# Optimization experiments

Hardware: AMD Instinct MI355X
Metric: run time of the kernel (lower is better)

Reference implementation:

```python
import jax, jax.numpy as jnp
import numpy as np

B, N, HID = 4, 2048, 1024
QKV, NH = 1024, 16
HD = QKV // NH


def setup_inputs() -> dict:
    key = jax.random.key(0)
    ks = jax.random.split(key, 5)
    s = 1.0 / np.sqrt(HID)
    x = jax.random.normal(ks[0], (B, N, HID), dtype=jnp.float32)
    Wq = jax.random.normal(ks[1], (HID, QKV), dtype=jnp.float32) * s
    Wk = jax.random.normal(ks[2], (HID, QKV), dtype=jnp.float32) * s
    Wv = jax.random.normal(ks[3], (HID, QKV), dtype=jnp.float32) * s
    Wo = jax.random.normal(ks[4], (QKV, HID), dtype=jnp.float32) * (1.0 / np.sqrt(QKV))
    return {"x": x, "Wq": Wq, "Wk": Wk, "Wv": Wv, "Wo": Wo}


def reference(x, Wq, Wk, Wv, Wo):
    # Projections: [B, N, QKV]
    q = x @ Wq
    k = x @ Wk
    v = x @ Wv
    # Split heads -> [B, NH, N, HD]
    def split(t):
        return t.reshape(B, N, NH, HD).transpose(0, 2, 1, 3)
    q, k, v = split(q), split(k), split(v)
    # NOTE: original scales by 1/sqrt(qkv_dim) (full dim), not head_dim
    q = q * (1.0 / jnp.sqrt(jnp.float32(QKV)))
    scores = jnp.einsum("bhqd,bhkd->bhqk", q, k)  # [B, NH, N, N]
    attn = jax.nn.softmax(scores, axis=-1)
    out = jnp.einsum("bhqk,bhkd->bhqd", attn, v)  # [B, NH, N, HD]
    out = out.transpose(0, 2, 1, 3).reshape(B, N, QKV)
    return out @ Wo
```

## Files before the change

### kernel.cpp

```cpp
#include <hip/hip_runtime.h>

typedef unsigned short u16;
typedef unsigned int u32;
typedef __attribute__((ext_vector_type(8))) short bf16x8;
typedef __attribute__((ext_vector_type(4))) float f32x4;
typedef __attribute__((ext_vector_type(16))) float f32x16;

#define L2E 1.44269504088896340736f

__device__ __forceinline__ u16 f2bf(float f) {
  unsigned u = __float_as_uint(f);
  u += 0x7FFF + ((u >> 16) & 1u);
  return (u16)(u >> 16);
}

__device__ __forceinline__ u32 cvtpk(float lo, float hi) {
  u32 r;
  asm("v_cvt_pk_bf16_f32 %0, %1, %2" : "=v"(r) : "v"(lo), "v"(hi));
  return r;
}

__device__ __forceinline__ void gload_lds16(const u16* g, u16* lds) {
  __builtin_amdgcn_global_load_lds(
      (const __attribute__((address_space(1))) void*)g,
      (__attribute__((address_space(3))) void*)lds, 16, 0, 0);
}

__global__ __launch_bounds__(256) void k_cvt(const float* __restrict__ in,
                                             u16* __restrict__ out) {
  const int i = (blockIdx.x * 256 + threadIdx.x) * 4;
  float4 a = *(const float4*)(in + i);
  ushort4 o;
  o.x = f2bf(a.x); o.y = f2bf(a.y); o.z = f2bf(a.z); o.w = f2bf(a.w);
  *(ushort4*)(out + i) = o;
}

__global__ __launch_bounds__(256) void k_tw(
    const float* __restrict__ w0, const float* __restrict__ w1,
    const float* __restrict__ w2, const float* __restrict__ w3,
    u16* __restrict__ o0, u16* __restrict__ o1,
    u16* __restrict__ o2, u16* __restrict__ o3) {
  __shared__ float t[64][65];
  const float* W = blockIdx.z == 0 ? w0 : blockIdx.z == 1 ? w1 : blockIdx.z == 2 ? w2 : w3;
  u16* O = blockIdx.z == 0 ? o0 : blockIdx.z == 1 ? o1 : blockIdx.z == 2 ? o2 : o3;
  const int nb = blockIdx.x * 64, kb = blockIdx.y * 64;
  const int lx = threadIdx.x & 63, ly = threadIdx.x >> 6;
  for (int r = ly; r < 64; r += 4)
    t[r][lx] = W[(size_t)(kb + r) * 1024 + nb + lx];
  __syncthreads();
  for (int r = ly; r < 64; r += 4)
    O[(size_t)(nb + r) * 1024 + kb + lx] = f2bf(t[lx][r]);
}

__device__ __forceinline__ void gemm_core(const u16* __restrict__ Ag,
                                          const u16* __restrict__ Bg,
                                          f32x4 acc[4][4]) {
  __shared__ u16 As[4096], Bs[4096];
  const int tid = threadIdx.x;
  const int lane = tid & 63, wv = tid >> 6;
  const size_t row0 = (size_t)blockIdx.y * 128;
  const size_t col0 = (size_t)blockIdx.x * 128;
  const int rA0 = wv * 32 + (lane >> 2);
  const int rA1 = rA0 + 16;
  const int kk = (lane & 3) * 8;
  const int wr = (wv >> 1) * 64, wc = (wv & 1) * 64;
  const int fr = lane & 15, fk = (lane >> 4) * 8;
#pragma unroll
  for (int m = 0; m < 4; m++)
#pragma unroll
    for (int n = 0; n < 4; n++)
      acc[m][n] = {0.f, 0.f, 0.f, 0.f};

  for (int kt = 0; kt < 32; kt++) {
    const int k0 = kt * 32;
    gload_lds16(Ag + (row0 + rA0) * 1024 + k0 + kk, &As[(wv * 2 + 0) * 512]);
    gload_lds16(Ag + (row0 + rA1) * 1024 + k0 + kk, &As[(wv * 2 + 1) * 512]);
    gload_lds16(Bg + (col0 + rA0) * 1024 + k0 + kk, &Bs[(wv * 2 + 0) * 512]);
    gload_lds16(Bg + (col0 + rA1) * 1024 + k0 + kk, &Bs[(wv * 2 + 1) * 512]);
    __syncthreads();
    bf16x8 af[4], bfr[4];
#pragma unroll
    for (int m = 0; m < 4; m++)
      af[m] = *(const bf16x8*)&As[(wr + m * 16 + fr) * 32 + fk];
#pragma unroll
    for (int n = 0; n < 4; n++)
      bfr[n] = *(const bf16x8*)&Bs[(wc + n * 16 + fr) * 32 + fk];
#pragma unroll
    for (int m = 0; m < 4; m++)
#pragma unroll
      for (int n = 0; n < 4; n++)
        acc[m][n] = __builtin_amdgcn_mfma_f32_16x16x32_bf16(af[m], bfr[n], acc[m][n], 0, 0, 0);
    __syncthreads();
  }
}

__global__ __launch_bounds__(256) void k_proj(
    const u16* __restrict__ xb, const u16* __restrict__ wqT,
    const u16* __restrict__ wkT, const u16* __restrict__ wvT,
    u16* __restrict__ q, u16* __restrict__ k, u16* __restrict__ v) {
  f32x4 acc[4][4];
  const int z = blockIdx.z;
  const u16* Bg = z == 0 ? wqT : z == 1 ? wkT : wvT;
  gemm_core(xb, Bg, acc);
  const int lane = threadIdx.x & 63, wv = threadIdx.x >> 6;
  const int wr = (wv >> 1) * 64, wc = (wv & 1) * 64;
  const int rb = blockIdx.y * 128 + wr + ((lane >> 4) * 4);
  const int cb = blockIdx.x * 128 + wc + (lane & 15);
#pragma unroll
  for (int m = 0; m < 4; m++) {
#pragma unroll
    for (int n = 0; n < 4; n++) {
      const int C = cb + n * 16;
      const int h = C >> 6, d = C & 63;
      if (z == 2) {
        const int R = rb + m * 16;
        const int b = R >> 11, nn = R & 2047;
        const int bh = b * 16 + h;
        ushort4 o;
        o.x = f2bf(acc[m][n][0]); o.y = f2bf(acc[m][n][1]);
        o.z = f2bf(acc[m][n][2]); o.w = f2bf(acc[m][n][3]);
        const size_t off = (size_t)bh * 131072 + (size_t)(nn >> 6) * 4096 +
                           ((nn & 63) >> 3) * 512 + d * 8 + (nn & 7);
        *(ushort4*)&v[off] = o;
      } else if (z == 1) {
#pragma unroll
        for (int i = 0; i < 4; i++) {
          const int R = rb + m * 16 + i;
          const int b = R >> 11, nn = R & 2047;
          const int bh = b * 16 + h;
          const size_t off = (size_t)bh * 131072 + (size_t)(nn >> 6) * 4096 +
                             (d >> 3) * 512 + (nn & 63) * 8 + (d & 7);
          k[off] = f2bf(acc[m][n][i]);
        }
      } else {
        const float s = 0.03125f * L2E;
#pragma unroll
        for (int i = 0; i < 4; i++) {
          const int R = rb + m * 16 + i;
          const int b = R >> 11, nn = R & 2047;
          q[(size_t)((b * 16 + h) * 2048 + nn) * 64 + d] = f2bf(acc[m][n][i] * s);
        }
      }
    }
  }
}

__global__ __launch_bounds__(256) void k_out(const u16* __restrict__ att,
                                             const u16* __restrict__ woT,
                                             float* __restrict__ out) {
  f32x4 acc[4][4];
  gemm_core(att, woT, acc);
  const int lane = threadIdx.x & 63, wv = threadIdx.x >> 6;
  const int wr = (wv >> 1) * 64, wc = (wv & 1) * 64;
  const int rb = blockIdx.y * 128 + wr + ((lane >> 4) * 4);
  const int cb = blockIdx.x * 128 + wc + (lane & 15);
#pragma unroll
  for (int m = 0; m < 4; m++)
#pragma unroll
    for (int n = 0; n < 4; n++)
#pragma unroll
      for (int i = 0; i < 4; i++)
        out[(size_t)(rb + m * 16 + i) * 1024 + cb + n * 16] = acc[m][n][i];
}

__global__ __launch_bounds__(256, 2) void k_attn(const u16* __restrict__ qg,
                                                 const u16* __restrict__ kg,
                                                 const u16* __restrict__ vg,
                                                 u16* __restrict__ att) {
  __shared__ u16 SM[16384];
  const int tid = threadIdx.x;
  const int lane = tid & 63, wv = tid >> 6;
  const int lo5 = lane & 31, hi = lane >> 5;
  const int bh = blockIdx.y;
  const int b = bh >> 4, h = bh & 15;
  const int q0w = blockIdx.x * 128 + wv * 32;
  const size_t qbase = (size_t)bh * 2048 * 64;
  const u16* kt0 = kg + (size_t)bh * 131072;
  const u16* vt0 = vg + (size_t)bh * 131072;

  bf16x8 qb[4];
  {
    const u16* qp = qg + qbase + (size_t)(q0w + lo5) * 64 + hi * 8;
#pragma unroll
    for (int db = 0; db < 4; db++) qb[db] = *(const bf16x8*)(qp + db * 16);
  }

  f32x16 o0, o1;
#pragma unroll
  for (int i = 0; i < 16; i++) { o0[i] = 0.f; o1[i] = 0.f; }
  float m_run = -3.0e38f;
  float l16[16];
#pragma unroll
  for (int i = 0; i < 16; i++) l16[i] = 0.f;

  gload_lds16(kt0 + (size_t)tid * 8, SM + wv * 512);
  gload_lds16(kt0 + (size_t)(256 + tid) * 8, SM + 2048 + wv * 512);
  gload_lds16(vt0 + (size_t)tid * 8, SM + 4096 + wv * 512);
  gload_lds16(vt0 + (size_t)(256 + tid) * 8, SM + 6144 + wv * 512);
  __syncthreads();

  int cur = 0;
  for (int t = 0; t < 32; t++) {
    {
      const int nt = (t + 1) & 31;
      const u16* ks = kt0 + (size_t)nt * 4096;
      const u16* vs = vt0 + (size_t)nt * 4096;
      u16* Kd = SM + (cur ^ 1) * 8192;
      gload_lds16(ks + (size_t)tid * 8, Kd + wv * 512);
      gload_lds16(ks + (size_t)(256 + tid) * 8, Kd + 2048 + wv * 512);
      gload_lds16(vs + (size_t)tid * 8, Kd + 4096 + wv * 512);
      gload_lds16(vs + (size_t)(256 + tid) * 8, Kd + 6144 + wv * 512);
    }

    const u16* Kc = SM + cur * 8192 + hi * 512 + lo5 * 8;
    const u16* Vc = Kc + 4096;

    f32x16 s0, s1;
#pragma unroll
    for (int i = 0; i < 16; i++) { s0[i] = 0.f; s1[i] = 0.f; }
    __builtin_amdgcn_s_setprio(1);
#pragma unroll
    for (int db = 0; db < 4; db++) {
      const bf16x8 k0 = *(const bf16x8*)&Kc[db * 1024];
      const bf16x8 k1 = *(const bf16x8*)&Kc[db * 1024 + 256];
      s0 = __builtin_amdgcn_mfma_f32_32x32x16_bf16(k0, qb[db], s0, 0, 0, 0);
      s1 = __builtin_amdgcn_mfma_f32_32x32x16_bf16(k1, qb[db], s1, 0, 0, 0);
    }
    __builtin_amdgcn_s_setprio(0);

    float tmx[16];
#pragma unroll
    for (int i = 0; i < 16; i++) tmx[i] = fmaxf(s0[i], s1[i]);
#pragma unroll
    for (int off = 8; off; off >>= 1)
#pragma unroll
      for (int i = 0; i < off; i++) tmx[i] = fmaxf(tmx[i], tmx[i + off]);
    const float tmax = fmaxf(tmx[0], __shfl_xor(tmx[0], 32, 64));

    const bool skip = __all(tmax - m_run <= 8.0f);
    if (!skip) {
      const float mnew = fmaxf(m_run, tmax);
      const float sc = __builtin_amdgcn_exp2f(m_run - mnew);
      m_run = mnew;
#pragma unroll
      for (int i = 0; i < 16; i++) {
        l16[i] *= sc; o0[i] *= sc; o1[i] *= sc;
      }
    }

    float p0[16], p1[16];
#pragma unroll
    for (int i = 0; i < 16; i++) {
      p0[i] = __builtin_amdgcn_exp2f(s0[i] - m_run);
      p1[i] = __builtin_amdgcn_exp2f(s1[i] - m_run);
      l16[i] += p0[i] + p1[i];
    }

    bf16x8 pa[4];
#pragma unroll
    for (int kh = 0; kh < 2; kh++) {
      const float* pp = kh ? p1 : p0;
#pragma unroll
      for (int kl = 0; kl < 2; kl++) {
        const int r0 = kl * 8;
        const u32 a0 = cvtpk(pp[r0 + 0], pp[r0 + 1]);
        const u32 a1 = cvtpk(pp[r0 + 2], pp[r0 + 3]);
        const u32 b0 = cvtpk(pp[r0 + 4], pp[r0 + 5]);
        const u32 b1 = cvtpk(pp[r0 + 6], pp[r0 + 7]);
        const u32 a0x = (u32)__shfl_xor((int)a0, 32, 64);
        const u32 a1x = (u32)__shfl_xor((int)a1, 32, 64);
        const u32 b0x = (u32)__shfl_xor((int)b0, 32, 64);
        const u32 b1x = (u32)__shfl_xor((int)b1, 32, 64);
        union { u32 w[4]; bf16x8 v; } U;
        U.w[0] = hi ? b0x : a0;
        U.w[1] = hi ? b1x : a1;
        U.w[2] = hi ? b0 : a0x;
        U.w[3] = hi ? b1 : a1x;
        pa[kh * 2 + kl] = U.v;
      }
    }

    __builtin_amdgcn_s_setprio(1);
#pragma unroll
    for (int ks = 0; ks < 4; ks++) {
      const bf16x8 v0 = *(const bf16x8*)&Vc[ks * 1024];
      const bf16x8 v1 = *(const bf16x8*)&Vc[ks * 1024 + 256];
      o0 = __builtin_amdgcn_mfma_f32_32x32x16_bf16(v0, pa[ks], o0, 0, 0, 0);
      o1 = __builtin_amdgcn_mfma_f32_32x32x16_bf16(v1, pa[ks], o1, 0, 0, 0);
    }
    __builtin_amdgcn_s_setprio(0);

    __syncthreads();
    cur ^= 1;
  }

  float ls[8];
#pragma unroll
  for (int i = 0; i < 8; i++) ls[i] = l16[i] + l16[i + 8];
#pragma unroll
  for (int off = 4; off; off >>= 1)
#pragma unroll
    for (int i = 0; i < off; i++) ls[i] += ls[i + off];
  const float lsum = ls[0] + __shfl_xor(ls[0], 32, 64);
  const float linv = 1.0f / lsum;

  u16* W = SM + wv * 2176;
#pragma unroll
  for (int r = 0; r < 16; r++) {
    const int dd = (r & 3) + 8 * (r >> 2) + 4 * hi;
    W[lo5 * 68 + dd] = f2bf(o0[r] * linv);
    W[lo5 * 68 + 32 + dd] = f2bf(o1[r] * linv);
  }
  const int q_loc = lane >> 1, dh = (lane & 1) * 32;
  u16* dst = att + (size_t)(b * 2048 + q0w + q_loc) * 1024 + h * 64 + dh;
#pragma unroll
  for (int c = 0; c < 4; c++) {
    bf16x8 val = *(const bf16x8*)&W[q_loc * 68 + dh + c * 8];
    *(bf16x8*)(dst + c * 8) = val;
  }
}

extern "C" void kernel_launch(void* const* d_in, const int* in_sizes, int n_in,
                              void* d_out, int out_size, void* d_ws, size_t ws_size,
                              hipStream_t stream) {
  const float* x  = (const float*)d_in[0];
  const float* Wq = (const float*)d_in[1];
  const float* Wk = (const float*)d_in[2];
  const float* Wv = (const float*)d_in[3];
  const float* Wo = (const float*)d_in[4];
  float* out = (float*)d_out;

  char* ws = (char*)d_ws;
  u16* xb  = (u16*)ws; ws += (size_t)8192 * 1024 * 2;
  u16* wqT = (u16*)ws; ws += (size_t)1024 * 1024 * 2;
  u16* wkT = (u16*)ws; ws += (size_t)1024 * 1024 * 2;
  u16* wvT = (u16*)ws; ws += (size_t)1024 * 1024 * 2;
  u16* woT = (u16*)ws; ws += (size_t)1024 * 1024 * 2;
  u16* qb  = (u16*)ws; ws += (size_t)8192 * 1024 * 2;
  u16* kb  = (u16*)ws; ws += (size_t)8192 * 1024 * 2;
  u16* vb  = (u16*)ws; ws += (size_t)8192 * 1024 * 2;
  u16* att = (u16*)ws; ws += (size_t)8192 * 1024 * 2;

  k_cvt<<<dim3(8192), dim3(256), 0, stream>>>(x, xb);
  k_tw<<<dim3(16, 16, 4), dim3(256), 0, stream>>>(Wq, Wk, Wv, Wo, wqT, wkT, wvT, woT);
  k_proj<<<dim3(8, 64, 3), dim3(256), 0, stream>>>(xb, wqT, wkT, wvT, qb, kb, vb);
  k_attn<<<dim3(16, 64), dim3(256), 0, stream>>>(qb, kb, vb, att);
  k_out<<<dim3(8, 64), dim3(256), 0, stream>>>(att, woT, out);
}
```

Baseline: 316.5 us.

## Rewrite projection and output GEMMs with pre-tiled operands and triple-buffered LDS pipeline

Adds a templated GEMM kernel with 512 threads and 128x256 tiles. It reads operands that the cvt, weight-transpose and attention-output kernels now write directly in a K-blocked tile layout, so each 16-byte global-to-LDS load is contiguous. A three-stage LDS ring replaces the synchronous load-barrier-compute loop, prefetching two k-steps ahead with waitcnt and barrier tuning and setprio around the MFMAs. This is meant to hide global-load latency and cut per-iteration barrier stalls in both GEMMs. In exchange it uses more LDS per block and gives a less flexible data layout.

Measured after the change: 283.9 us. 10.3% less time.

```diff
diff --git a/kernel.cpp b/kernel.cpp
--- a/kernel.cpp
+++ b/kernel.cpp
@@ -8,6 +8,7 @@
 
 #define L2E 1.44269504088896340736f
 
+
 __device__ __forceinline__ u16 f2bf(float f) {
   unsigned u = __float_as_uint(f);
   u += 0x7FFF + ((u >> 16) & 1u);
@@ -29,138 +30,172 @@
 __global__ __launch_bounds__(256) void k_cvt(const float* __restrict__ in,
                                              u16* __restrict__ out) {
   const int i = (blockIdx.x * 256 + threadIdx.x) * 4;
+  const int n = i >> 10, kk = i & 1023;
   float4 a = *(const float4*)(in + i);
   ushort4 o;
   o.x = f2bf(a.x); o.y = f2bf(a.y); o.z = f2bf(a.z); o.w = f2bf(a.w);
-  *(ushort4*)(out + i) = o;
+  const size_t off = (size_t)(kk >> 5) * 262144 + (size_t)(n >> 7) * 4096 +
+                     ((kk >> 3) & 3) * 1024 + (n & 127) * 8 + (kk & 7);
+  *(ushort4*)(out + off) = o;
 }
 
 __global__ __launch_bounds__(256) void k_tw(
     const float* __restrict__ w0, const float* __restrict__ w1,
     const float* __restrict__ w2, const float* __restrict__ w3,
-    u16* __restrict__ o0, u16* __restrict__ o1,
-    u16* __restrict__ o2, u16* __restrict__ o3) {
+    u16* __restrict__ wqkv, u16* __restrict__ wo) {
   __shared__ float t[64][65];
-  const float* W = blockIdx.z == 0 ? w0 : blockIdx.z == 1 ? w1 : blockIdx.z == 2 ? w2 : w3;
-  u16* O = blockIdx.z == 0 ? o0 : blockIdx.z == 1 ? o1 : blockIdx.z == 2 ? o2 : o3;
+  const int z = blockIdx.z;
+  const float* W = z == 0 ? w0 : z == 1 ? w1 : z == 2 ? w2 : w3;
   const int nb = blockIdx.x * 64, kb = blockIdx.y * 64;
   const int lx = threadIdx.x & 63, ly = threadIdx.x >> 6;
   for (int r = ly; r < 64; r += 4)
     t[r][lx] = W[(size_t)(kb + r) * 1024 + nb + lx];
   __syncthreads();
-  for (int r = ly; r < 64; r += 4)
-    O[(size_t)(nb + r) * 1024 + kb + lx] = f2bf(t[lx][r]);
-}
-
-__device__ __forceinline__ void gemm_core(const u16* __restrict__ Ag,
-                                          const u16* __restrict__ Bg,
-                                          f32x4 acc[4][4]) {
-  __shared__ u16 As[4096], Bs[4096];
-  const int tid = threadIdx.x;
-  const int lane = tid & 63, wv = tid >> 6;
-  const size_t row0 = (size_t)blockIdx.y * 128;
-  const size_t col0 = (size_t)blockIdx.x * 128;
-  const int rA0 = wv * 32 + (lane >> 2);
-  const int rA1 = rA0 + 16;
-  const int kk = (lane & 3) * 8;
-  const int wr = (wv >> 1) * 64, wc = (wv & 1) * 64;
-  const int fr = lane & 15, fk = (lane >> 4) * 8;
+  const int kk = kb + lx;
+  for (int r = ly; r < 64; r += 4) {
+    const int n = nb + r;
+    const u16 val = f2bf(t[lx][r]);
+    if (z < 3) {
+      const size_t off = (size_t)(kk >> 5) * 98304 + (size_t)(z * 8 + (n >> 7)) * 4096 +
+                         ((kk >> 3) & 3) * 1024 + (n & 127) * 8 + (kk & 7);
+      wqkv[off] = val;
+    } else {
+      const size_t off = (size_t)(kk >> 5) * 32768 + (size_t)(n >> 7) * 4096 +
+                         ((kk >> 3) & 3) * 1024 + (n & 127) * 8 + (kk & 7);
+      wo[off] = val;
+    }
+  }
+}
+
+template <int MODE>
+__global__ __launch_bounds__(512) void k_mm(const u16* __restrict__ Ag,
+                                            const u16* __restrict__ Bg,
+                                            u16* __restrict__ qo,
+                                            u16* __restrict__ ko,
+                                            u16* __restrict__ vo,
+                                            float* __restrict__ outp) {
+  __shared__ u16 SM[3 * 12288];
+  const int tid = threadIdx.x, lane = tid & 63, wv = tid >> 6;
+  const int wm = wv >> 2, wn = wv & 3;
+  const int fr = lane & 15, hi = lane >> 4;
+  const int bn = blockIdx.x, bm = blockIdx.y;
+  const int PKB = (MODE == 0) ? 98304 : 32768;
+  const u16* Asrc = Ag + (size_t)bm * 4096;
+  const u16* Bsrc = Bg + (size_t)(bn * 2) * 4096;
+
+  f32x4 acc[4][4];
 #pragma unroll
   for (int m = 0; m < 4; m++)
 #pragma unroll
-    for (int n = 0; n < 4; n++)
-      acc[m][n] = {0.f, 0.f, 0.f, 0.f};
-
-  for (int kt = 0; kt < 32; kt++) {
-    const int k0 = kt * 32;
-    gload_lds16(Ag + (row0 + rA0) * 1024 + k0 + kk, &As[(wv * 2 + 0) * 512]);
-    gload_lds16(Ag + (row0 + rA1) * 1024 + k0 + kk, &As[(wv * 2 + 1) * 512]);
-    gload_lds16(Bg + (col0 + rA0) * 1024 + k0 + kk, &Bs[(wv * 2 + 0) * 512]);
-    gload_lds16(Bg + (col0 + rA1) * 1024 + k0 + kk, &Bs[(wv * 2 + 1) * 512]);
-    __syncthreads();
+    for (int n = 0; n < 4; n++) acc[m][n] = {0.f, 0.f, 0.f, 0.f};
+
+  int aoff[4], boff[4];
+#pragma unroll
+  for (int m = 0; m < 4; m++)
+    aoff[m] = hi * 1024 + (wm * 64 + m * 16 + fr) * 8;
+#pragma unroll
+  for (int n = 0; n < 4; n++) {
+    const int col = wn * 64 + n * 16 + fr;
+    boff[n] = 4096 + (col >> 7) * 4096 + hi * 1024 + (col & 127) * 8;
+  }
+
+#pragma unroll
+  for (int p = 0; p < 2; p++) {
+    u16* D = SM + p * 12288;
+    const u16* As = Asrc + (size_t)p * 262144;
+    const u16* Bs = Bsrc + (size_t)p * PKB;
+    gload_lds16(As + tid * 8, D + wv * 512);
+    gload_lds16(Bs + tid * 8, D + 4096 + wv * 512);
+    gload_lds16(Bs + 4096 + tid * 8, D + 8192 + wv * 512);
+  }
+  asm volatile("s_waitcnt vmcnt(3)" ::: "memory");
+  __builtin_amdgcn_s_barrier();
+  __builtin_amdgcn_sched_barrier(0);
+
+  int cur = 0, stg = 2;
+  for (int t = 0; t < 32; t++) {
+    {
+      const int nt = (t + 2) & 31;
+      u16* D = SM + stg * 12288;
+      const u16* As = Asrc + (size_t)nt * 262144;
+      const u16* Bs = Bsrc + (size_t)nt * PKB;
+      gload_lds16(As + tid * 8, D + wv * 512);
+      gload_lds16(Bs + tid * 8, D + 4096 + wv * 512);
+      gload_lds16(Bs + 4096 + tid * 8, D + 8192 + wv * 512);
+    }
+    const u16* buf = SM + cur * 12288;
     bf16x8 af[4], bfr[4];
 #pragma unroll
-    for (int m = 0; m < 4; m++)
-      af[m] = *(const bf16x8*)&As[(wr + m * 16 + fr) * 32 + fk];
-#pragma unroll
-    for (int n = 0; n < 4; n++)
-      bfr[n] = *(const bf16x8*)&Bs[(wc + n * 16 + fr) * 32 + fk];
+    for (int m = 0; m < 4; m++) af[m] = *(const bf16x8*)&buf[aoff[m]];
+#pragma unroll
+    for (int n = 0; n < 4; n++) bfr[n] = *(const bf16x8*)&buf[boff[n]];
+    asm volatile("s_waitcnt lgkmcnt(0)" ::: "memory");
+    __builtin_amdgcn_sched_barrier(0);
+    __builtin_amdgcn_s_setprio(1);
 #pragma unroll
     for (int m = 0; m < 4; m++)
 #pragma unroll
       for (int n = 0; n < 4; n++)
         acc[m][n] = __builtin_amdgcn_mfma_f32_16x16x32_bf16(af[m], bfr[n], acc[m][n], 0, 0, 0);
-    __syncthreads();
-  }
-}
-
-__global__ __launch_bounds__(256) void k_proj(
-    const u16* __restrict__ xb, const u16* __restrict__ wqT,
-    const u16* __restrict__ wkT, const u16* __restrict__ wvT,
-    u16* __restrict__ q, u16* __restrict__ k, u16* __restrict__ v) {
-  f32x4 acc[4][4];
-  const int z = blockIdx.z;
-  const u16* Bg = z == 0 ? wqT : z == 1 ? wkT : wvT;
-  gemm_core(xb, Bg, acc);
-  const int lane = threadIdx.x & 63, wv = threadIdx.x >> 6;
-  const int wr = (wv >> 1) * 64, wc = (wv & 1) * 64;
-  const int rb = blockIdx.y * 128 + wr + ((lane >> 4) * 4);
-  const int cb = blockIdx.x * 128 + wc + (lane & 15);
-#pragma unroll
-  for (int m = 0; m < 4; m++) {
-#pragma unroll
-    for (int n = 0; n < 4; n++) {
-      const int C = cb + n * 16;
-      const int h = C >> 6, d = C & 63;
-      if (z == 2) {
-        const int R = rb + m * 16;
-        const int b = R >> 11, nn = R & 2047;
-        const int bh = b * 16 + h;
-        ushort4 o;
-        o.x = f2bf(acc[m][n][0]); o.y = f2bf(acc[m][n][1]);
-        o.z = f2bf(acc[m][n][2]); o.w = f2bf(acc[m][n][3]);
-        const size_t off = (size_t)bh * 131072 + (size_t)(nn >> 6) * 4096 +
-                           ((nn & 63) >> 3) * 512 + d * 8 + (nn & 7);
-        *(ushort4*)&v[off] = o;
-      } else if (z == 1) {
-#pragma unroll
-        for (int i = 0; i < 4; i++) {
-          const int R = rb + m * 16 + i;
+    __builtin_amdgcn_s_setprio(0);
+    asm volatile("s_waitcnt vmcnt(3)" ::: "memory");
+    __builtin_amdgcn_s_barrier();
+    __builtin_amdgcn_sched_barrier(0);
+    cur = (cur == 2) ? 0 : cur + 1;
+    stg = (stg == 2) ? 0 : stg + 1;
+  }
+
+  const int rb = bm * 128 + wm * 64 + hi * 4;
+  if (MODE == 1) {
+#pragma unroll
+    for (int m = 0; m < 4; m++)
+#pragma unroll
+      for (int n = 0; n < 4; n++) {
+        const int C = bn * 256 + wn * 64 + n * 16 + fr;
+#pragma unroll
+        for (int i = 0; i < 4; i++)
+          outp[(size_t)(rb + m * 16 + i) * 1024 + C] = acc[m][n][i];
+      }
+  } else {
+    const int z = bn >> 2;
+#pragma unroll
+    for (int m = 0; m < 4; m++) {
+#pragma unroll
+      for (int n = 0; n < 4; n++) {
+        const int C = (bn & 3) * 256 + wn * 64 + n * 16 + fr;
+        const int h = C >> 6, d = C & 63;
+        if (z == 2) {
+          const int R = rb + m * 16;
           const int b = R >> 11, nn = R & 2047;
           const int bh = b * 16 + h;
+          ushort4 o;
+          o.x = f2bf(acc[m][n][0]); o.y = f2bf(acc[m][n][1]);
+          o.z = f2bf(acc[m][n][2]); o.w = f2bf(acc[m][n][3]);
           const size_t off = (size_t)bh * 131072 + (size_t)(nn >> 6) * 4096 +
-                             (d >> 3) * 512 + (nn & 63) * 8 + (d & 7);
-          k[off] = f2bf(acc[m][n][i]);
-        }
-      } else {
-        const float s = 0.03125f * L2E;
-#pragma unroll
-        for (int i = 0; i < 4; i++) {
-          const int R = rb + m * 16 + i;
-          const int b = R >> 11, nn = R & 2047;
-          q[(size_t)((b * 16 + h) * 2048 + nn) * 64 + d] = f2bf(acc[m][n][i] * s);
+                             ((nn & 63) >> 3) * 512 + d * 8 + (nn & 7);
+          *(ushort4*)&vo[off] = o;
+        } else if (z == 1) {
+#pragma unroll
+          for (int i = 0; i < 4; i++) {
+            const int R = rb + m * 16 + i;
+            const int b = R >> 11, nn = R & 2047;
+            const int bh = b * 16 + h;
+            const size_t off = (size_t)bh * 131072 + (size_t)(nn >> 6) * 4096 +
+                               (d >> 3) * 512 + (nn & 63) * 8 + (d & 7);
+            ko[off] = f2bf(acc[m][n][i]);
+          }
+        } else {
+          const float s = 0.03125f * L2E;
+#pragma unroll
+          for (int i = 0; i < 4; i++) {
+            const int R = rb + m * 16 + i;
+            const int b = R >> 11, nn = R & 2047;
+            qo[(size_t)((b * 16 + h) * 2048 + nn) * 64 + d] = f2bf(acc[m][n][i] * s);
+          }
         }
       }
     }
   }
-}
-
-__global__ __launch_bounds__(256) void k_out(const u16* __restrict__ att,
-                                             const u16* __restrict__ woT,
-                                             float* __restrict__ out) {
-  f32x4 acc[4][4];
-  gemm_core(att, woT, acc);
-  const int lane = threadIdx.x & 63, wv = threadIdx.x >> 6;
-  const int wr = (wv >> 1) * 64, wc = (wv & 1) * 64;
-  const int rb = blockIdx.y * 128 + wr + ((lane >> 4) * 4);
-  const int cb = blockIdx.x * 128 + wc + (lane & 15);
-#pragma unroll
-  for (int m = 0; m < 4; m++)
-#pragma unroll
-    for (int n = 0; n < 4; n++)
-#pragma unroll
-      for (int i = 0; i < 4; i++)
-        out[(size_t)(rb + m * 16 + i) * 1024 + cb + n * 16] = acc[m][n][i];
 }
 
 __global__ __launch_bounds__(256, 2) void k_attn(const u16* __restrict__ qg,
@@ -243,9 +278,7 @@
       const float sc = __builtin_amdgcn_exp2f(m_run - mnew);
       m_run = mnew;
 #pragma unroll
-      for (int i = 0; i < 16; i++) {
-        l16[i] *= sc; o0[i] *= sc; o1[i] *= sc;
-      }
+      for (int i = 0; i < 16; i++) { l16[i] *= sc; o0[i] *= sc; o1[i] *= sc; }
     }
 
     float p0[16], p1[16];
@@ -312,11 +345,14 @@
     W[lo5 * 68 + 32 + dd] = f2bf(o1[r] * linv);
   }
   const int q_loc = lane >> 1, dh = (lane & 1) * 32;
-  u16* dst = att + (size_t)(b * 2048 + q0w + q_loc) * 1024 + h * 64 + dh;
+  const int nrow = b * 2048 + q0w + q_loc;
+  const size_t rowpart = (size_t)(nrow >> 7) * 4096 + (nrow & 127) * 8;
 #pragma unroll
   for (int c = 0; c < 4; c++) {
+    const int kk = h * 64 + dh + c * 8;
     bf16x8 val = *(const bf16x8*)&W[q_loc * 68 + dh + c * 8];
-    *(bf16x8*)(dst + c * 8) = val;
+    const size_t off = (size_t)(kk >> 5) * 262144 + rowpart + ((kk >> 3) & 3) * 1024;
+    *(bf16x8*)(att + off) = val;
   }
 }
 
@@ -331,19 +367,17 @@
   float* out = (float*)d_out;
 
   char* ws = (char*)d_ws;
-  u16* xb  = (u16*)ws; ws += (size_t)8192 * 1024 * 2;
-  u16* wqT = (u16*)ws; ws += (size_t)1024 * 1024 * 2;
-  u16* wkT = (u16*)ws; ws += (size_t)1024 * 1024 * 2;
-  u16* wvT = (u16*)ws; ws += (size_t)1024 * 1024 * 2;
-  u16* woT = (u16*)ws; ws += (size_t)1024 * 1024 * 2;
-  u16* qb  = (u16*)ws; ws += (size_t)8192 * 1024 * 2;
-  u16* kb  = (u16*)ws; ws += (size_t)8192 * 1024 * 2;
-  u16* vb  = (u16*)ws; ws += (size_t)8192 * 1024 * 2;
-  u16* att = (u16*)ws; ws += (size_t)8192 * 1024 * 2;
+  u16* xb   = (u16*)ws; ws += (size_t)8192 * 1024 * 2;
+  u16* wqkv = (u16*)ws; ws += (size_t)3072 * 1024 * 2;
+  u16* woT  = (u16*)ws; ws += (size_t)1024 * 1024 * 2;
+  u16* qb   = (u16*)ws; ws += (size_t)8192 * 1024 * 2;
+  u16* kb   = (u16*)ws; ws += (size_t)8192 * 1024 * 2;
+  u16* vb   = (u16*)ws; ws += (size_t)8192 * 1024 * 2;
+  u16* att  = (u16*)ws; ws += (size_t)8192 * 1024 * 2;
 
   k_cvt<<<dim3(8192), dim3(256), 0, stream>>>(x, xb);
-  k_tw<<<dim3(16, 16, 4), dim3(256), 0, stream>>>(Wq, Wk, Wv, Wo, wqT, wkT, wvT, woT);
-  k_proj<<<dim3(8, 64, 3), dim3(256), 0, stream>>>(xb, wqT, wkT, wvT, qb, kb, vb);
+  k_tw<<<dim3(16, 16, 4), dim3(256), 0, stream>>>(Wq, Wk, Wv, Wo, wqkv, woT);
+  k_mm<0><<<dim3(12, 64), dim3(512), 0, stream>>>(xb, wqkv, qb, kb, vb, nullptr);
   k_attn<<<dim3(16, 64), dim3(256), 0, stream>>>(qb, kb, vb, att);
-  k_out<<<dim3(8, 64), dim3(256), 0, stream>>>(att, woT, out);
-}
+  k_mm<1><<<dim3(4, 64), dim3(512), 0, stream>>>(att, woT, nullptr, nullptr, nullptr, out);
+}
```
